# Kernel optimization log

Measured on AMD Instinct MI355X. Metric: run time of the kernel, lower is better.

Reference implementation:

```python
import jax, jax.numpy as jnp
import numpy as np

H = 64          # hidden_dim
NH = 4          # n_heads
DH = H // NH
F_OWN = 40      # own feature dim
FA = 24         # ally feature dim
FE = 24         # enemy feature dim
NAL = 15        # n_allies
NEN = 16        # n_enemies
BS = 2048       # episode batch
NAG = 16        # n_agents
BN = BS * NAG
AMOVE = 6       # normal (move) actions
HYPER_OUT = F_OWN * H + H + 4


def setup_inputs():
    key = jax.random.key(0)
    ks = jax.random.split(key, 32)
    g = lambda k, sh, s=1.0: jax.random.normal(k, sh, dtype=jnp.float32) * s
    inv = lambda d: float(1.0 / np.sqrt(d))
    return {
        "own_raw": g(ks[0], (BN, 1, F_OWN)),
        "ally_raw": g(ks[1], (BN, NAL, FA)),
        "enemy_raw": g(ks[2], (BN, NEN, FE)),
        "hidden_state": g(ks[3], (BN, H)),
        "hyp_W1": g(ks[4], (F_OWN, H), inv(F_OWN)),
        "hyp_b1": jnp.zeros((H,), jnp.float32),
        "hyp_W2": g(ks[5], (H, HYPER_OUT), 0.01 * inv(H)),  # torch init mul_(0.01)
        "hyp_b2": jnp.zeros((HYPER_OUT,), jnp.float32),
        "Wa": g(ks[6], (FA, H), inv(FA)), "ba": jnp.zeros((H,), jnp.float32),
        "We": g(ks[7], (FE, H), inv(FE)), "be": jnp.zeros((H,), jnp.float32),
        "aWq": g(ks[8], (H, H), inv(H)), "aWk": g(ks[9], (H, H), inv(H)),
        "aWv": g(ks[10], (H, H), inv(H)), "aWo": g(ks[11], (H, H), inv(H)),
        "eWq": g(ks[12], (H, H), inv(H)), "eWk": g(ks[13], (H, H), inv(H)),
        "eWv": g(ks[14], (H, H), inv(H)), "eWo": g(ks[15], (H, H), inv(H)),
        "gru_Wih": g(ks[16], (3 * H, 3 * H), inv(3 * H)),
        "gru_Whh": g(ks[17], (H, 3 * H), inv(H)),
        "gru_bih": jnp.zeros((3 * H,), jnp.float32),
        "gru_bhh": jnp.zeros((3 * H,), jnp.float32),
        "Wm": g(ks[18], (H, AMOVE), inv(H)), "bm": jnp.zeros((AMOVE,), jnp.float32),
        "WzK": g(ks[19], (H, H), inv(H)),
        "WEK": g(ks[20], (H, H), inv(H)),
        "bs": BS,
    }


def _mha(q_in, kv, mask, Wq, Wk, Wv, Wo):
    # masked multi-head cross attention: q_in [B,H], kv [B,n,H], mask [B,n] bool
    B, n = kv.shape[0], kv.shape[1]
    q = (q_in @ Wq).reshape(B, NH, DH)
    k = (kv @ Wk).reshape(B, n, NH, DH)
    v = (kv @ Wv).reshape(B, n, NH, DH)
    scores = jnp.einsum('bhd,bnhd->bhn', q, k) * float(1.0 / np.sqrt(DH))
    scores = jnp.where(mask[:, None, :], scores, -1e9)
    attn = jax.nn.softmax(scores, axis=-1)
    out = jnp.einsum('bhn,bnhd->bhd', attn, v).reshape(B, H)
    return out @ Wo


def reference(own_raw, ally_raw, enemy_raw, hidden_state,
              hyp_W1, hyp_b1, hyp_W2, hyp_b2,
              Wa, ba, We, be,
              aWq, aWk, aWv, aWo, eWq, eWk, eWv, eWo,
              gru_Wih, gru_Whh, gru_bih, gru_bhh,
              Wm, bm, WzK, WEK, bs):
    Bn = own_raw.shape[0]
    ally_mask = jnp.any(ally_raw != 0, axis=-1)    # ~all(x==0)
    enemy_mask = jnp.any(enemy_raw != 0, axis=-1)
    own_vec = own_raw[:, 0, :]                     # [Bn, F_OWN]
    # hypernet: per-agent own-embedding weights + bias (last 4 outputs unused, as in source)
    h_out = jax.nn.relu(own_vec @ hyp_W1 + hyp_b1) @ hyp_W2 + hyp_b2
    W_flat = h_out[:, :F_OWN * H].reshape(Bn, F_OWN, H)
    b_own = h_out[:, F_OWN * H:F_OWN * H + H]
    own_e = jnp.einsum('bf,bfh->bh', own_vec, W_flat) + b_own
    ally_e = ally_raw @ Wa + ba
    enemy_e = enemy_raw @ We + be
    zA = _mha(own_e, ally_e, ally_mask, aWq, aWk, aWv, aWo)
    zE = _mha(own_e, enemy_e, enemy_mask, eWq, eWk, eWv, eWo)
    u_cat = jnp.concatenate([own_e, zA, zE], axis=-1)  # [Bn, 3H]
    # GRUCell (torch semantics)
    gx = u_cat @ gru_Wih + gru_bih
    gh = hidden_state @ gru_Whh + gru_bhh
    xr, xz, xn = jnp.split(gx, 3, axis=-1)
    hr, hz, hn = jnp.split(gh, 3, axis=-1)
    r = jax.nn.sigmoid(xr + hr)
    zg = jax.nn.sigmoid(xz + hz)
    ncand = jnp.tanh(xn + r * hn)
    z = (1.0 - zg) * ncand + zg * hidden_state
    logits_move = z @ Wm + bm
    zk = z @ WzK
    Ek = enemy_e @ WEK
    logits_shoot = jnp.einsum('bd,bmd->bm', zk, Ek)
    Q = jnp.concatenate([logits_move, logits_shoot], axis=-1)[:, None, :]
    return Q, z.reshape(bs, -1, H)
```

## Files before the change

kernel.cpp:

```cpp
#include <hip/hip_runtime.h>
#include <hip/hip_bf16.h>
#include <math.h>

#define TB 32
#define LOG2E 1.44269504f

typedef float f32x4 __attribute__((ext_vector_type(4)));
typedef _Float16 f16x8 __attribute__((ext_vector_type(8)));
typedef _Float16 f16x4 __attribute__((ext_vector_type(4)));
typedef _Float16 f16x2 __attribute__((ext_vector_type(2)));

#define OFF_W1T  344064
#define OFF_WOA  352256
#define OFF_WOE  360448
#define OFF_VBA  368640
#define OFF_VBE  372736
#define OFF_GA   376832
#define OFF_GE   393216
#define OFF_GIH  409600
#define OFF_GHH  483328
#define OFF_GBS  507904
#define OFF_GBH  508672
#define OFF_BHD  508928

#define MFH(a, b, c) __builtin_amdgcn_mfma_f32_16x16x32_f16((a), (b), (c), 0, 0, 0)

__device__ inline float dot2(f16x2 a, f16x2 b, float c) {
#if __has_builtin(__builtin_amdgcn_fdot2)
  return __builtin_amdgcn_fdot2(a, b, c, false);
#else
  return c + (float)a[0] * (float)b[0] + (float)a[1] * (float)b[1];
#endif
}
__device__ inline f16x2 pk2(float x, float y) {
  f16x2 r; r[0] = (_Float16)x; r[1] = (_Float16)y; return r;
}

__global__ __launch_bounds__(256)
void prep_kernel(const float* __restrict__ hyp_W1, const float* __restrict__ hyp_b1,
                 const float* __restrict__ hyp_W2, const float* __restrict__ hyp_b2,
                 const float* __restrict__ Wa, const float* __restrict__ ba,
                 const float* __restrict__ We, const float* __restrict__ be,
                 const float* __restrict__ aWq, const float* __restrict__ aWk,
                 const float* __restrict__ aWv, const float* __restrict__ aWo,
                 const float* __restrict__ eWq, const float* __restrict__ eWk,
                 const float* __restrict__ eWv, const float* __restrict__ eWo,
                 const float* __restrict__ gWih, const float* __restrict__ gWhh,
                 const float* __restrict__ gbih, const float* __restrict__ gbhh,
                 const float* __restrict__ WzK, const float* __restrict__ WEK,
                 const float* __restrict__ Wm,
                 void* __restrict__ ws)
{
  const int b = blockIdx.x, t = threadIdx.x;
  if (b < 42) {
    _Float16* o = (_Float16*)ws;
    for (int i = t; i < 4096; i += 256) {
      int h = i >> 6, k = i & 63;
      float v;
      if (b < 40)       v = hyp_W2[(size_t)k * 2628 + b * 64 + h];
      else if (b == 40) v = hyp_W2[(size_t)k * 2628 + 2560 + h];
      else              v = (k < 40) ? hyp_b2[k * 64 + h]
                             : (k == 40 ? hyp_b2[2560 + h] : 0.0f);
      o[b * 4096 + i] = (_Float16)v;
    }
  } else if (b == 42) {
    _Float16* o = (_Float16*)((char*)ws + OFF_W1T);
    for (int i = t; i < 4096; i += 256) {
      int h = i >> 6, k = i & 63;
      float v = (k < 40) ? hyp_W1[k * 64 + h] : (k == 40 ? hyp_b1[h] : 0.0f);
      o[i] = (_Float16)v;
    }
  } else if (b == 43 || b == 44) {
    const float* M = (b == 43) ? aWo : eWo;
    _Float16* o = (_Float16*)((char*)ws + (b == 43 ? OFF_WOA : OFF_WOE));
    for (int i = t; i < 4096; i += 256)
      o[i] = (_Float16)M[(i & 63) * 64 + (i >> 6)];
  } else if (b == 45 || b == 46) {
    const float* Wemb = (b == 45) ? Wa : We;
    const float* bemb = (b == 45) ? ba : be;
    const float* Wv   = (b == 45) ? aWv : eWv;
    _Float16* o = (_Float16*)((char*)ws + (b == 45 ? OFF_VBA : OFF_VBE));
    for (int i = t; i < 2048; i += 256) {
      int h = i >> 5, k = i & 31;
      float v = 0.f;
      if (k < 24)       { for (int d = 0; d < 64; ++d) v += Wemb[k * 64 + d] * Wv[d * 64 + h]; }
      else if (k == 24) { for (int d = 0; d < 64; ++d) v += bemb[d] * Wv[d * 64 + h]; }
      o[i] = (_Float16)v;
    }
  } else if (b == 47 || b == 48) {
    const float* Wemb = (b == 47) ? Wa : We;
    const float* bemb = (b == 47) ? ba : be;
    const float* Wk   = (b == 47) ? aWk : eWk;
    const float* Wq   = (b == 47) ? aWq : eWq;
    _Float16* o = (_Float16*)((char*)ws + (b == 47 ? OFF_GA : OFF_GE));
    __shared__ float sKb[25 * 64];
    for (int i = t; i < 1600; i += 256) {
      int k = i >> 6, c = i & 63;
      float v = 0.f;
      if (k < 24)  { for (int d = 0; d < 64; ++d) v += Wemb[k * 64 + d] * Wk[d * 64 + c]; }
      else         { for (int d = 0; d < 64; ++d) v += bemb[d] * Wk[d * 64 + c]; }
      sKb[i] = v;
    }
    __syncthreads();
    for (int i = t; i < 8192; i += 256) {
      int col = i >> 6, d = i & 63;
      int h = col >> 5, kk = col & 31;
      float v = 0.f;
      if (kk < 25)
        for (int dh = 0; dh < 16; ++dh)
          v += Wq[d * 64 + h * 16 + dh] * sKb[kk * 64 + h * 16 + dh];
      o[i] = (_Float16)(v * 0.25f * LOG2E);
    }
  } else if (b == 49) {
    _Float16* o = (_Float16*)((char*)ws + OFF_GIH);
    for (int i = t; i < 36864; i += 256) {
      int d = i / 192, c = i - d * 192;
      o[c * 192 + d] = (_Float16)gWih[i];
    }
  } else if (b == 50) {
    _Float16* o = (_Float16*)((char*)ws + OFF_GHH);
    for (int i = t; i < 12288; i += 256) {
      int d = i / 192, c = i - d * 192;
      o[c * 64 + d] = (_Float16)gWhh[i];
    }
  } else if (b == 51) {
    float* gbS = (float*)((char*)ws + OFF_GBS);
    float* gbH = (float*)((char*)ws + OFF_GBH);
    if (t < 192) gbS[t] = gbih[t] + (t < 128 ? gbhh[t] : 0.0f);
    if (t < 64)  gbH[t] = gbhh[128 + t];
  } else if (b == 52) {
    __shared__ float sWsK[24 * 64];
    __shared__ float sbw[64];
    _Float16* o = (_Float16*)((char*)ws + OFF_BHD);
    for (int i = t; i < 1536; i += 256) {
      int j = i >> 6, h = i & 63;
      float v = 0.f;
      for (int c = 0; c < 64; ++c) v += We[j * 64 + c] * WEK[c * 64 + h];
      sWsK[i] = v;
    }
    if (t < 64) {
      float v = 0.f;
      for (int c = 0; c < 64; ++c) v += be[c] * WEK[c * 64 + t];
      sbw[t] = v;
    }
    __syncthreads();
    for (int i = t; i < 2048; i += 256) {
      int col = i >> 6, c = i & 63;
      float v = 0.f;
      if (col < 24)       { for (int d = 0; d < 64; ++d) v += WzK[c * 64 + d] * sWsK[col * 64 + d]; }
      else if (col == 24) { for (int d = 0; d < 64; ++d) v += WzK[c * 64 + d] * sbw[d]; }
      else if (col < 31)  v = Wm[c * 6 + (col - 25)];
      o[i] = (_Float16)v;
    }
  }
}

#define SCORE_BODY(Q0,Q1,Q2,Q3,Q4,Q5,WP,SCV)                                  \
  {                                                                            \
    unsigned orv =                                                             \
      ((Q0.x!=0.f)|(Q0.y!=0.f)|(Q0.z!=0.f)|(Q0.w!=0.f)|                        \
       (Q1.x!=0.f)|(Q1.y!=0.f)|(Q1.z!=0.f)|(Q1.w!=0.f)|                        \
       (Q2.x!=0.f)|(Q2.y!=0.f)|(Q2.z!=0.f)|(Q2.w!=0.f)|                        \
       (Q3.x!=0.f)|(Q3.y!=0.f)|(Q3.z!=0.f)|(Q3.w!=0.f)|                        \
       (Q4.x!=0.f)|(Q4.y!=0.f)|(Q4.z!=0.f)|(Q4.w!=0.f)|                        \
       (Q5.x!=0.f)|(Q5.y!=0.f)|(Q5.z!=0.f)|(Q5.w!=0.f)) ? 1u : 0u;             \
    f16x2 r0 = pk2(Q0.x,Q0.y), r1 = pk2(Q0.z,Q0.w);                            \
    f16x2 r2 = pk2(Q1.x,Q1.y), r3 = pk2(Q1.z,Q1.w);                            \
    f16x2 r4 = pk2(Q2.x,Q2.y), r5 = pk2(Q2.z,Q2.w);                            \
    f16x2 r6 = pk2(Q3.x,Q3.y), r7 = pk2(Q3.z,Q3.w);                            \
    f16x2 r8 = pk2(Q4.x,Q4.y), r9 = pk2(Q4.z,Q4.w);                            \
    f16x2 r10 = pk2(Q5.x,Q5.y), r11 = pk2(Q5.z,Q5.w);                          \
    _Pragma("unroll")                                                          \
    for (int h = 0; h < 4; ++h) {                                              \
      const _Float16* wq = (WP) + h * 32;                                      \
      float a = (float)wq[24];                                                 \
      a = dot2(r0,  *(const f16x2*)(wq + 0),  a);                              \
      a = dot2(r1,  *(const f16x2*)(wq + 2),  a);                              \
      a = dot2(r2,  *(const f16x2*)(wq + 4),  a);                              \
      a = dot2(r3,  *(const f16x2*)(wq + 6),  a);                              \
      a = dot2(r4,  *(const f16x2*)(wq + 8),  a);                              \
      a = dot2(r5,  *(const f16x2*)(wq + 10), a);                              \
      a = dot2(r6,  *(const f16x2*)(wq + 12), a);                              \
      a = dot2(r7,  *(const f16x2*)(wq + 14), a);                              \
      a = dot2(r8,  *(const f16x2*)(wq + 16), a);                              \
      a = dot2(r9,  *(const f16x2*)(wq + 18), a);                              \
      a = dot2(r10, *(const f16x2*)(wq + 20), a);                              \
      a = dot2(r11, *(const f16x2*)(wq + 22), a);                              \
      SCV[h] = orv ? a : -1.0e9f;                                              \
    }                                                                          \
  }

__global__ __launch_bounds__(256, 4)
void agent_kernel(
    const float* __restrict__ own_raw, const float* __restrict__ ally_raw,
    const float* __restrict__ enemy_raw, const float* __restrict__ hidden,
    const float* __restrict__ bm,
    const void* __restrict__ ws,
    float* __restrict__ out, int BN)
{
  __shared__ __align__(16) char s_all[37632];
  _Float16* s_u16 = (_Float16*)s_all;
  char*     sR2   = s_all + 12544;
  _Float16* s_own16 = (_Float16*)sR2;
  _Float16* s_ownT  = (_Float16*)(sR2 + 3328);
  _Float16* s_h116  = (_Float16*)(sR2 + 5888);
  _Float16* s_w0    = (_Float16*)sR2;
  _Float16* s_w1    = (_Float16*)(sR2 + 8320);
  _Float16* s_pp0   = (_Float16*)(sR2 + 16640);
  _Float16* s_pp1   = (_Float16*)(sR2 + 20864);
  _Float16* s_att0  = (_Float16*)sR2;
  _Float16* s_att1  = (_Float16*)(sR2 + 8320);
  _Float16* s_hid16 = (_Float16*)(sR2 + 16640);
  _Float16* s_z16   = (_Float16*)sR2;
  _Float16* s_t16   = (_Float16*)(sR2 + 4352);
  float*    s_q     = (float*)(sR2 + 8320);

  const int tid = threadIdx.x;
  const int bs0 = blockIdx.x * TB;
  const int l   = tid & 63;
  const int wv  = tid >> 6;
  const int lr  = l & 15;
  const int oct = l >> 4;
  const int s8  = tid >> 3;
  const int sh  = tid & 7;

  const f16x8 ZERO8F = {0,0,0,0,0,0,0,0};
  f16x8 ONE8F = ZERO8F; ONE8F[0] = (_Float16)1.0f;
  const f32x4 ZERO4 = {0.f, 0.f, 0.f, 0.f};

  for (int i = tid; i < 640; i += 256) {
    int ss = i / 20, c = i - ss * 20;
    float2 v = *(const float2*)(own_raw + (size_t)(bs0 + ss) * 40 + c * 2);
    *(f16x2*)(s_own16 + ss * 52 + c * 2) = pk2(v.x, v.y);
  }
  for (int i = tid; i < 1280; i += 256) {
    int f = i >> 5, s2 = i & 31;
    s_ownT[i] = (_Float16)own_raw[(size_t)(bs0 + s2) * 40 + f];
  }
  __syncthreads();

  {
    const _Float16* w1t = (const _Float16*)((const char*)ws + OFF_W1T);
    f16x8 b0 = *(const f16x8*)(w1t + (wv * 16 + lr) * 64 + oct * 8);
    f16x8 b1 = *(const f16x8*)(w1t + (wv * 16 + lr) * 64 + 32 + oct * 8);
    #pragma unroll
    for (int rt = 0; rt < 2; ++rt) {
      f16x8 a0 = *(const f16x8*)(s_own16 + (rt * 16 + lr) * 52 + oct * 8);
      f16x8 a1;
      if (oct == 0)      a1 = *(const f16x8*)(s_own16 + (rt * 16 + lr) * 52 + 32);
      else if (oct == 1) a1 = ONE8F;
      else               a1 = ZERO8F;
      f32x4 acc = ZERO4;
      acc = MFH(a0, b0, acc);
      acc = MFH(a1, b1, acc);
      #pragma unroll
      for (int j = 0; j < 4; ++j)
        s_h116[(rt * 16 + oct * 4 + j) * 68 + wv * 16 + lr] = (_Float16)fmaxf(acc[j], 0.f);
    }
  }
  __syncthreads();

  {
    const _Float16* bb = (const _Float16*)ws + (size_t)(wv * 16 + lr) * 64 + oct * 8;
    f16x8 h0f0 = *(const f16x8*)(s_h116 + lr * 68 + oct * 8);
    f16x8 h1f0 = *(const f16x8*)(s_h116 + lr * 68 + 32 + oct * 8);
    f16x8 h0f1 = *(const f16x8*)(s_h116 + (16 + lr) * 68 + oct * 8);
    f16x8 h1f1 = *(const f16x8*)(s_h116 + (16 + lr) * 68 + 32 + oct * 8);
    f32x4 acc0 = ZERO4, acc1 = ZERO4;
    #pragma unroll 4
    for (int f = 0; f < 40; ++f) {
      f16x8 b0 = *(const f16x8*)(bb + (size_t)f * 4096);
      f16x8 b1 = *(const f16x8*)(bb + (size_t)f * 4096 + 32);
      f32x4 y0 = MFH(h0f0, b0, ZERO4); y0 = MFH(h1f0, b1, y0);
      f32x4 y1 = MFH(h0f1, b0, ZERO4); y1 = MFH(h1f1, b1, y1);
      f16x4 ov0 = *(const f16x4*)(s_ownT + f * 32 + oct * 4);
      f16x4 ov1 = *(const f16x4*)(s_ownT + f * 32 + 16 + oct * 4);
      #pragma unroll
      for (int j = 0; j < 4; ++j) {
        acc0[j] += (float)ov0[j] * y0[j];
        acc1[j] += (float)ov1[j] * y1[j];
      }
    }
    f32x4 aD0 = ZERO4, aD1 = ZERO4;
    {
      f16x8 b0 = *(const f16x8*)(bb + (size_t)40 * 4096);
      f16x8 b1 = *(const f16x8*)(bb + (size_t)40 * 4096 + 32);
      aD0 = MFH(h0f0, b0, aD0); aD0 = MFH(h1f0, b1, aD0);
      aD1 = MFH(h0f1, b0, aD1); aD1 = MFH(h1f1, b1, aD1);
    }
    {
      f16x8 b0 = *(const f16x8*)(bb + (size_t)41 * 4096);
      f16x8 b1 = *(const f16x8*)(bb + (size_t)41 * 4096 + 32);
      #pragma unroll
      for (int rt = 0; rt < 2; ++rt) {
        f16x8 a0 = *(const f16x8*)(s_own16 + (rt * 16 + lr) * 52 + oct * 8);
        f16x8 a1;
        if (oct == 0)      a1 = *(const f16x8*)(s_own16 + (rt * 16 + lr) * 52 + 32);
        else if (oct == 1) a1 = ONE8F;
        else               a1 = ZERO8F;
        if (rt) { aD1 = MFH(a0, b0, aD1); aD1 = MFH(a1, b1, aD1); }
        else    { aD0 = MFH(a0, b0, aD0); aD0 = MFH(a1, b1, aD0); }
      }
    }
    #pragma unroll
    for (int j = 0; j < 4; ++j) {
      s_u16[(oct * 4 + j) * 196 + wv * 16 + lr]      = (_Float16)(acc0[j] + aD0[j]);
      s_u16[(16 + oct * 4 + j) * 196 + wv * 16 + lr] = (_Float16)(acc1[j] + aD1[j]);
    }
  }
  __syncthreads();

  {
    f16x8 a00 = *(const f16x8*)(s_u16 + lr * 196 + oct * 8);
    f16x8 a10 = *(const f16x8*)(s_u16 + lr * 196 + 32 + oct * 8);
    f16x8 a01 = *(const f16x8*)(s_u16 + (16 + lr) * 196 + oct * 8);
    f16x8 a11 = *(const f16x8*)(s_u16 + (16 + lr) * 196 + 32 + oct * 8);
    #pragma unroll
    for (int side = 0; side < 2; ++side) {
      const _Float16* gT = (const _Float16*)((const char*)ws + (side ? OFF_GE : OFF_GA));
      _Float16* wDst = side ? s_w1 : s_w0;
      #pragma unroll
      for (int t2 = 0; t2 < 2; ++t2) {
        int col = wv * 32 + t2 * 16 + lr;
        f16x8 b0 = *(const f16x8*)(gT + col * 64 + oct * 8);
        f16x8 b1 = *(const f16x8*)(gT + col * 64 + 32 + oct * 8);
        f32x4 ac0 = ZERO4, ac1 = ZERO4;
        ac0 = MFH(a00, b0, ac0); ac0 = MFH(a10, b1, ac0);
        ac1 = MFH(a01, b0, ac1); ac1 = MFH(a11, b1, ac1);
        #pragma unroll
        for (int j = 0; j < 4; ++j) {
          wDst[(oct * 4 + j) * 130 + col]      = (_Float16)ac0[j];
          wDst[(16 + oct * 4 + j) * 130 + col] = (_Float16)ac1[j];
        }
      }
    }
  }
  __syncthreads();

  {
    #pragma unroll
    for (int side = 0; side < 2; ++side) {
      const int n_ent = side ? 16 : 15;
      const int rstr  = side ? 384 : 360;
      const float* rawg = side ? enemy_raw : ally_raw;
      const _Float16* wp = (side ? s_w1 : s_w0) + s8 * 130;
      _Float16* pp = side ? s_pp1 : s_pp0;

      const int n1 = (sh + 8 < n_ent) ? (sh + 8) : (n_ent - 1);
      const float* rp0 = rawg + (size_t)(bs0 + s8) * rstr + sh * 24;
      const float* rp1 = rawg + (size_t)(bs0 + s8) * rstr + n1 * 24;
      float4 qa0 = *(const float4*)(rp0);      float4 qa1 = *(const float4*)(rp0 + 4);
      float4 qa2 = *(const float4*)(rp0 + 8);  float4 qa3 = *(const float4*)(rp0 + 12);
      float4 qa4 = *(const float4*)(rp0 + 16); float4 qa5 = *(const float4*)(rp0 + 20);
      float4 qb0 = *(const float4*)(rp1);      float4 qb1 = *(const float4*)(rp1 + 4);
      float4 qb2 = *(const float4*)(rp1 + 8);  float4 qb3 = *(const float4*)(rp1 + 12);
      float4 qb4 = *(const float4*)(rp1 + 16); float4 qb5 = *(const float4*)(rp1 + 20);

      f32x4 sc0, sc1;
      SCORE_BODY(qa0, qa1, qa2, qa3, qa4, qa5, wp, sc0);
      SCORE_BODY(qb0, qb1, qb2, qb3, qb4, qb5, wp, sc1);
      if (sh + 8 >= n_ent) {
        #pragma unroll
        for (int h = 0; h < 4; ++h) sc1[h] = -2.0e9f;
      }
      f32x4 m, lsum, p0v, p1v;
      #pragma unroll
      for (int h = 0; h < 4; ++h) m[h] = fmaxf(sc0[h], sc1[h]);
      #pragma unroll
      for (int d = 1; d < 8; d <<= 1) {
        #pragma unroll
        for (int h = 0; h < 4; ++h) m[h] = fmaxf(m[h], __shfl_xor(m[h], d));
      }
      #pragma unroll
      for (int h = 0; h < 4; ++h) {
        p0v[h] = __builtin_exp2f(sc0[h] - m[h]);
        p1v[h] = __builtin_exp2f(sc1[h] - m[h]);
        lsum[h] = p0v[h] + p1v[h];
      }
      #pragma unroll
      for (int d = 1; d < 8; d <<= 1) {
        #pragma unroll
        for (int h = 0; h < 4; ++h) lsum[h] += __shfl_xor(lsum[h], d);
      }
      f32x4 rl;
      #pragma unroll
      for (int h = 0; h < 4; ++h) rl[h] = __builtin_amdgcn_rcpf(lsum[h]);
      {
        f16x4 pk;
        #pragma unroll
        for (int h = 0; h < 4; ++h) pk[h] = (_Float16)(p0v[h] * rl[h]);
        *(f16x4*)(pp + sh * 132 + s8 * 4) = pk;
      }
      if (sh + 8 < n_ent) {
        f16x4 pk;
        #pragma unroll
        for (int h = 0; h < 4; ++h) pk[h] = (_Float16)(p1v[h] * rl[h]);
        *(f16x4*)(pp + (sh + 8) * 132 + s8 * 4) = pk;
      }
    }
  }
  __syncthreads();

  {
    #pragma unroll
    for (int side = 0; side < 2; ++side) {
      const int n_ent = side ? 16 : 15;
      const int rstr  = side ? 384 : 360;
      const float* rawg = side ? enemy_raw : ally_raw;
      const _Float16* vbT = (const _Float16*)((const char*)ws + (side ? OFF_VBE : OFF_VBA));
      const _Float16* pp = side ? s_pp1 : s_pp0;
      _Float16* attD = side ? s_att1 : s_att0;

      f16x8 vbF = *(const f16x8*)(vbT + (wv * 16 + lr) * 32 + oct * 8);
      const float* rpv0 = rawg + (size_t)(bs0 + lr) * rstr + oct * 8;
      const float* rpv1 = rawg + (size_t)(bs0 + 16 + lr) * rstr + oct * 8;
      f32x4 oac0 = ZERO4, oac1 = ZERO4;
      #pragma unroll
      for (int i = 0; i < 16; ++i) {
        if (i >= n_ent) break;
        _Float16 pw0 = pp[i * 132 + lr * 4 + wv];
        _Float16 pw1 = pp[i * 132 + (16 + lr) * 4 + wv];
        f16x8 fr0, fr1;
        if (oct < 3) {
          float4 a = *(const float4*)(rpv0 + i * 24);
          float4 b = *(const float4*)(rpv0 + i * 24 + 4);
          fr0[0] = (_Float16)a.x * pw0; fr0[1] = (_Float16)a.y * pw0;
          fr0[2] = (_Float16)a.z * pw0; fr0[3] = (_Float16)a.w * pw0;
          fr0[4] = (_Float16)b.x * pw0; fr0[5] = (_Float16)b.y * pw0;
          fr0[6] = (_Float16)b.z * pw0; fr0[7] = (_Float16)b.w * pw0;
          float4 c = *(const float4*)(rpv1 + i * 24);
          float4 d = *(const float4*)(rpv1 + i * 24 + 4);
          fr1[0] = (_Float16)c.x * pw1; fr1[1] = (_Float16)c.y * pw1;
          fr1[2] = (_Float16)c.z * pw1; fr1[3] = (_Float16)c.w * pw1;
          fr1[4] = (_Float16)d.x * pw1; fr1[5] = (_Float16)d.y * pw1;
          fr1[6] = (_Float16)d.z * pw1; fr1[7] = (_Float16)d.w * pw1;
        } else {
          fr0 = ZERO8F; fr0[0] = pw0;
          fr1 = ZERO8F; fr1[0] = pw1;
        }
        oac0 = MFH(fr0, vbF, oac0);
        oac1 = MFH(fr1, vbF, oac1);
      }
      if (side == 0) __syncthreads();
      #pragma unroll
      for (int j = 0; j < 4; ++j) {
        attD[(oct * 4 + j) * 68 + wv * 16 + lr]      = (_Float16)oac0[j];
        attD[(16 + oct * 4 + j) * 68 + wv * 16 + lr] = (_Float16)oac1[j];
      }
    }
  }
  __syncthreads();

  {
    #pragma unroll
    for (int side = 0; side < 2; ++side) {
      const _Float16* woT = (const _Float16*)((const char*)ws + (side ? OFF_WOE : OFF_WOA));
      const _Float16* attS = side ? s_att1 : s_att0;
      f16x8 b0 = *(const f16x8*)(woT + (wv * 16 + lr) * 64 + oct * 8);
      f16x8 b1 = *(const f16x8*)(woT + (wv * 16 + lr) * 64 + 32 + oct * 8);
      #pragma unroll
      for (int rt = 0; rt < 2; ++rt) {
        f16x8 a0 = *(const f16x8*)(attS + (rt * 16 + lr) * 68 + oct * 8);
        f16x8 a1 = *(const f16x8*)(attS + (rt * 16 + lr) * 68 + 32 + oct * 8);
        f32x4 oa = ZERO4;
        oa = MFH(a0, b0, oa);
        oa = MFH(a1, b1, oa);
        #pragma unroll
        for (int j = 0; j < 4; ++j)
          s_u16[(rt * 16 + oct * 4 + j) * 196 + 64 + side * 64 + wv * 16 + lr] = (_Float16)oa[j];
      }
    }
    for (int i = tid; i < 1024; i += 256) {
      int ss = i >> 5, c = i & 31;
      float2 v = *(const float2*)(hidden + (size_t)(bs0 + ss) * 64 + c * 2);
      *(f16x2*)(s_hid16 + ss * 68 + c * 2) = pk2(v.x, v.y);
    }
  }
  __syncthreads();

  {
    const _Float16* ihT = (const _Float16*)((const char*)ws + OFF_GIH);
    const _Float16* hhT = (const _Float16*)((const char*)ws + OFF_GHH);
    const float* gbS = (const float*)((const char*)ws + OFF_GBS);
    const float* gbH = (const float*)((const char*)ws + OFF_GBH);
    f32x4 aX0[2] = {ZERO4, ZERO4}, aX1[2] = {ZERO4, ZERO4};
    f32x4 aX2[2] = {ZERO4, ZERO4}, aH2[2] = {ZERO4, ZERO4};
    #pragma unroll
    for (int st = 0; st < 6; ++st) {
      f16x8 uf0 = *(const f16x8*)(s_u16 + lr * 196 + st * 32 + oct * 8);
      f16x8 uf1 = *(const f16x8*)(s_u16 + (16 + lr) * 196 + st * 32 + oct * 8);
      f16x8 b0 = *(const f16x8*)(ihT + ((wv    ) * 16 + lr) * 192 + st * 32 + oct * 8);
      f16x8 b1 = *(const f16x8*)(ihT + ((wv + 4) * 16 + lr) * 192 + st * 32 + oct * 8);
      f16x8 b2 = *(const f16x8*)(ihT + ((wv + 8) * 16 + lr) * 192 + st * 32 + oct * 8);
      aX0[0] = MFH(uf0, b0, aX0[0]);  aX0[1] = MFH(uf1, b0, aX0[1]);
      aX1[0] = MFH(uf0, b1, aX1[0]);  aX1[1] = MFH(uf1, b1, aX1[1]);
      aX2[0] = MFH(uf0, b2, aX2[0]);  aX2[1] = MFH(uf1, b2, aX2[1]);
    }
    #pragma unroll
    for (int st = 0; st < 2; ++st) {
      f16x8 hf0 = *(const f16x8*)(s_hid16 + lr * 68 + st * 32 + oct * 8);
      f16x8 hf1 = *(const f16x8*)(s_hid16 + (16 + lr) * 68 + st * 32 + oct * 8);
      f16x8 b0 = *(const f16x8*)(hhT + ((wv    ) * 16 + lr) * 64 + st * 32 + oct * 8);
      f16x8 b1 = *(const f16x8*)(hhT + ((wv + 4) * 16 + lr) * 64 + st * 32 + oct * 8);
      f16x8 b2 = *(const f16x8*)(hhT + ((wv + 8) * 16 + lr) * 64 + st * 32 + oct * 8);
      aX0[0] = MFH(hf0, b0, aX0[0]);  aX0[1] = MFH(hf1, b0, aX0[1]);
      aX1[0] = MFH(hf0, b1, aX1[0]);  aX1[1] = MFH(hf1, b1, aX1[1]);
      aH2[0] = MFH(hf0, b2, aH2[0]);  aH2[1] = MFH(hf1, b2, aH2[1]);
    }
    const int c0 = wv * 16 + lr;
    float bb0 = gbS[c0], bb1 = gbS[c0 + 64], bb2 = gbS[c0 + 128], bbh = gbH[c0];
    #pragma unroll
    for (int rt = 0; rt < 2; ++rt) {
      #pragma unroll
      for (int j = 0; j < 4; ++j) {
        int row = rt * 16 + oct * 4 + j;
        float xr = aX0[rt][j] + bb0;
        float xz = aX1[rt][j] + bb1;
        float xn = aX2[rt][j] + bb2;
        float hn = aH2[rt][j] + bbh;
        float r  = __builtin_amdgcn_rcpf(1.f + __builtin_exp2f(-xr * LOG2E));
        float zg = __builtin_amdgcn_rcpf(1.f + __builtin_exp2f(-xz * LOG2E));
        float ta = xn + r * hn;
        float nc = 1.f - 2.f * __builtin_amdgcn_rcpf(1.f + __builtin_exp2f(2.f * LOG2E * ta));
        float hv = (float)s_hid16[row * 68 + c0];
        s_z16[row * 68 + c0] = (_Float16)((1.f - zg) * nc + zg * hv);
      }
    }
  }
  __syncthreads();

  {
    const _Float16* bhT = (const _Float16*)((const char*)ws + OFF_BHD);
    const int rt = wv >> 1;
    const int col = (wv & 1) * 16 + lr;
    f16x8 a0 = *(const f16x8*)(s_z16 + (rt * 16 + lr) * 68 + oct * 8);
    f16x8 a1 = *(const f16x8*)(s_z16 + (rt * 16 + lr) * 68 + 32 + oct * 8);
    f16x8 b0 = *(const f16x8*)(bhT + col * 64 + oct * 8);
    f16x8 b1 = *(const f16x8*)(bhT + col * 64 + 32 + oct * 8);
    f32x4 td = ZERO4;
    td = MFH(a0, b0, td);
    td = MFH(a1, b1, td);
    #pragma unroll
    for (int j = 0; j < 4; ++j) {
      int row = rt * 16 + oct * 4 + j;
      if (col < 25)      s_t16[row * 26 + col] = (_Float16)td[j];
      else if (col < 31) s_q[row * 22 + (col - 25)] = td[j] + bm[col - 25];
    }
  }
  __syncthreads();
  {
    const _Float16* tp = s_t16 + s8 * 26;
    #pragma unroll
    for (int e = 0; e < 2; ++e) {
      int m = sh + e * 8;
      const float* er = enemy_raw + (size_t)(bs0 + s8) * 384 + m * 24;
      float acc2 = (float)tp[24];
      #pragma unroll
      for (int k4 = 0; k4 < 6; ++k4) {
        float4 r4 = *(const float4*)(er + k4 * 4);
        acc2 += r4.x * (float)tp[k4*4]   + r4.y * (float)tp[k4*4+1]
              + r4.z * (float)tp[k4*4+2] + r4.w * (float)tp[k4*4+3];
      }
      s_q[s8 * 22 + 6 + m] = acc2;
    }
  }
  __syncthreads();
  for (int i = tid; i < 704; i += 256)
    out[(size_t)bs0 * 22 + i] = s_q[i];
  for (int i = tid; i < 2048; i += 256)
    out[(size_t)BN * 22 + (size_t)bs0 * 64 + i] = (float)s_z16[(i >> 6) * 68 + (i & 63)];
}

extern "C" void kernel_launch(void* const* d_in, const int* in_sizes, int n_in,
                              void* d_out, int out_size, void* d_ws, size_t ws_size,
                              hipStream_t stream) {
  (void)n_in; (void)out_size; (void)ws_size;
  const float* own_raw   = (const float*)d_in[0];
  const float* ally_raw  = (const float*)d_in[1];
  const float* enemy_raw = (const float*)d_in[2];
  const float* hidden    = (const float*)d_in[3];
  const float* hyp_W1    = (const float*)d_in[4];
  const float* hyp_b1    = (const float*)d_in[5];
  const float* hyp_W2    = (const float*)d_in[6];
  const float* hyp_b2    = (const float*)d_in[7];
  const float* Wa        = (const float*)d_in[8];
  const float* ba        = (const float*)d_in[9];
  const float* We        = (const float*)d_in[10];
  const float* be        = (const float*)d_in[11];
  const float* aWq       = (const float*)d_in[12];
  const float* aWk       = (const float*)d_in[13];
  const float* aWv       = (const float*)d_in[14];
  const float* aWo       = (const float*)d_in[15];
  const float* eWq       = (const float*)d_in[16];
  const float* eWk       = (const float*)d_in[17];
  const float* eWv       = (const float*)d_in[18];
  const float* eWo       = (const float*)d_in[19];
  const float* gWih      = (const float*)d_in[20];
  const float* gWhh      = (const float*)d_in[21];
  const float* gbih      = (const float*)d_in[22];
  const float* gbhh      = (const float*)d_in[23];
  const float* Wm        = (const float*)d_in[24];
  const float* bm        = (const float*)d_in[25];
  const float* WzK       = (const float*)d_in[26];
  const float* WEK       = (const float*)d_in[27];
  int BN = in_sizes[0] / 40;
  int blocks = BN / TB;

  hipLaunchKernelGGL(prep_kernel, dim3(53), dim3(256), 0, stream,
                     hyp_W1, hyp_b1, hyp_W2, hyp_b2, Wa, ba, We, be,
                     aWq, aWk, aWv, aWo, eWq, eWk, eWv, eWo,
                     gWih, gWhh, gbih, gbhh, WzK, WEK, Wm, d_ws);
  hipLaunchKernelGGL(agent_kernel, dim3(blocks), dim3(256), 0, stream,
                     own_raw, ally_raw, enemy_raw, hidden, bm,
                     d_ws, (float*)d_out, BN);
}
```

Before: 146.7 us.

## Repad LDS strides, vectorize score dots, and make entity loops branch-free

Row strides of every shared-memory tile are padded to multiples of 8 halfs (52→56, 68→72, 130→136, 196→200), so 16-byte f16x8 loads are aligned and bank mapping changes. The attention score code now loads each weight row once as f16x8 vectors and reuses it for both entity slots. The final shoot logits convert the enemy rows to fp16 and use packed dot2 instead of scalar fp32 multiply-adds. The entity loop in the value aggregation loses its early break and uses clamped indices, and the probability scaling is done in fp32 before packing. One barrier is moved and s_q is relocated to a new region, which changes synchronisation and adds a small amount of LDS.

```diff
diff --git a/kernel.cpp b/kernel.cpp
--- a/kernel.cpp
+++ b/kernel.cpp
@@ -35,6 +35,30 @@
 __device__ inline f16x2 pk2(float x, float y) {
   f16x2 r; r[0] = (_Float16)x; r[1] = (_Float16)y; return r;
 }
+
+#define SV2(W, q) __builtin_shufflevector((W), (W), 2*(q), 2*(q)+1)
+
+#define CVT12(Q0,Q1,Q2,Q3,Q4,Q5,R) \
+  f16x2 R##_0=pk2(Q0.x,Q0.y), R##_1=pk2(Q0.z,Q0.w), \
+        R##_2=pk2(Q1.x,Q1.y), R##_3=pk2(Q1.z,Q1.w), \
+        R##_4=pk2(Q2.x,Q2.y), R##_5=pk2(Q2.z,Q2.w), \
+        R##_6=pk2(Q3.x,Q3.y), R##_7=pk2(Q3.z,Q3.w), \
+        R##_8=pk2(Q4.x,Q4.y), R##_9=pk2(Q4.z,Q4.w), \
+        R##_10=pk2(Q5.x,Q5.y), R##_11=pk2(Q5.z,Q5.w)
+
+#define ORV6(Q0,Q1,Q2,Q3,Q4,Q5) \
+  ((Q0.x!=0.f)|(Q0.y!=0.f)|(Q0.z!=0.f)|(Q0.w!=0.f)| \
+   (Q1.x!=0.f)|(Q1.y!=0.f)|(Q1.z!=0.f)|(Q1.w!=0.f)| \
+   (Q2.x!=0.f)|(Q2.y!=0.f)|(Q2.z!=0.f)|(Q2.w!=0.f)| \
+   (Q3.x!=0.f)|(Q3.y!=0.f)|(Q3.z!=0.f)|(Q3.w!=0.f)| \
+   (Q4.x!=0.f)|(Q4.y!=0.f)|(Q4.z!=0.f)|(Q4.w!=0.f)| \
+   (Q5.x!=0.f)|(Q5.y!=0.f)|(Q5.z!=0.f)|(Q5.w!=0.f))
+
+#define DOT12(R, WA, WB, WC, BIAS) \
+  dot2(R##_11, SV2(WC,3), dot2(R##_10, SV2(WC,2), dot2(R##_9, SV2(WC,1), dot2(R##_8, SV2(WC,0), \
+  dot2(R##_7,  SV2(WB,3), dot2(R##_6,  SV2(WB,2), dot2(R##_5, SV2(WB,1), dot2(R##_4, SV2(WB,0), \
+  dot2(R##_3,  SV2(WA,3), dot2(R##_2,  SV2(WA,2), dot2(R##_1, SV2(WA,1), dot2(R##_0, SV2(WA,0), \
+  (BIAS)))))))))))))
 
 __global__ __launch_bounds__(256)
 void prep_kernel(const float* __restrict__ hyp_W1, const float* __restrict__ hyp_b1,
@@ -155,41 +179,6 @@
   }
 }
 
-#define SCORE_BODY(Q0,Q1,Q2,Q3,Q4,Q5,WP,SCV)                                  \
-  {                                                                            \
-    unsigned orv =                                                             \
-      ((Q0.x!=0.f)|(Q0.y!=0.f)|(Q0.z!=0.f)|(Q0.w!=0.f)|                        \
-       (Q1.x!=0.f)|(Q1.y!=0.f)|(Q1.z!=0.f)|(Q1.w!=0.f)|                        \
-       (Q2.x!=0.f)|(Q2.y!=0.f)|(Q2.z!=0.f)|(Q2.w!=0.f)|                        \
-       (Q3.x!=0.f)|(Q3.y!=0.f)|(Q3.z!=0.f)|(Q3.w!=0.f)|                        \
-       (Q4.x!=0.f)|(Q4.y!=0.f)|(Q4.z!=0.f)|(Q4.w!=0.f)|                        \
-       (Q5.x!=0.f)|(Q5.y!=0.f)|(Q5.z!=0.f)|(Q5.w!=0.f)) ? 1u : 0u;             \
-    f16x2 r0 = pk2(Q0.x,Q0.y), r1 = pk2(Q0.z,Q0.w);                            \
-    f16x2 r2 = pk2(Q1.x,Q1.y), r3 = pk2(Q1.z,Q1.w);                            \
-    f16x2 r4 = pk2(Q2.x,Q2.y), r5 = pk2(Q2.z,Q2.w);                            \
-    f16x2 r6 = pk2(Q3.x,Q3.y), r7 = pk2(Q3.z,Q3.w);                            \
-    f16x2 r8 = pk2(Q4.x,Q4.y), r9 = pk2(Q4.z,Q4.w);                            \
-    f16x2 r10 = pk2(Q5.x,Q5.y), r11 = pk2(Q5.z,Q5.w);                          \
-    _Pragma("unroll")                                                          \
-    for (int h = 0; h < 4; ++h) {                                              \
-      const _Float16* wq = (WP) + h * 32;                                      \
-      float a = (float)wq[24];                                                 \
-      a = dot2(r0,  *(const f16x2*)(wq + 0),  a);                              \
-      a = dot2(r1,  *(const f16x2*)(wq + 2),  a);                              \
-      a = dot2(r2,  *(const f16x2*)(wq + 4),  a);                              \
-      a = dot2(r3,  *(const f16x2*)(wq + 6),  a);                              \
-      a = dot2(r4,  *(const f16x2*)(wq + 8),  a);                              \
-      a = dot2(r5,  *(const f16x2*)(wq + 10), a);                              \
-      a = dot2(r6,  *(const f16x2*)(wq + 12), a);                              \
-      a = dot2(r7,  *(const f16x2*)(wq + 14), a);                              \
-      a = dot2(r8,  *(const f16x2*)(wq + 16), a);                              \
-      a = dot2(r9,  *(const f16x2*)(wq + 18), a);                              \
-      a = dot2(r10, *(const f16x2*)(wq + 20), a);                              \
-      a = dot2(r11, *(const f16x2*)(wq + 22), a);                              \
-      SCV[h] = orv ? a : -1.0e9f;                                              \
-    }                                                                          \
-  }
-
 __global__ __launch_bounds__(256, 4)
 void agent_kernel(
     const float* __restrict__ own_raw, const float* __restrict__ ally_raw,
@@ -198,22 +187,22 @@
     const void* __restrict__ ws,
     float* __restrict__ out, int BN)
 {
-  __shared__ __align__(16) char s_all[37632];
+  __shared__ __align__(16) char s_all[38656];
   _Float16* s_u16 = (_Float16*)s_all;
-  char*     sR2   = s_all + 12544;
+  char*     sR2   = s_all + 12800;
   _Float16* s_own16 = (_Float16*)sR2;
-  _Float16* s_ownT  = (_Float16*)(sR2 + 3328);
-  _Float16* s_h116  = (_Float16*)(sR2 + 5888);
+  _Float16* s_ownT  = (_Float16*)(sR2 + 3584);
+  _Float16* s_h116  = (_Float16*)(sR2 + 6144);
   _Float16* s_w0    = (_Float16*)sR2;
-  _Float16* s_w1    = (_Float16*)(sR2 + 8320);
-  _Float16* s_pp0   = (_Float16*)(sR2 + 16640);
-  _Float16* s_pp1   = (_Float16*)(sR2 + 20864);
+  _Float16* s_w1    = (_Float16*)(sR2 + 8704);
+  _Float16* s_pp0   = (_Float16*)(sR2 + 17408);
+  _Float16* s_pp1   = (_Float16*)(sR2 + 21632);
   _Float16* s_att0  = (_Float16*)sR2;
-  _Float16* s_att1  = (_Float16*)(sR2 + 8320);
-  _Float16* s_hid16 = (_Float16*)(sR2 + 16640);
+  _Float16* s_att1  = (_Float16*)(sR2 + 8704);
+  _Float16* s_hid16 = (_Float16*)(sR2 + 17408);
   _Float16* s_z16   = (_Float16*)sR2;
-  _Float16* s_t16   = (_Float16*)(sR2 + 4352);
-  float*    s_q     = (float*)(sR2 + 8320);
+  _Float16* s_t16   = (_Float16*)(sR2 + 4608);
+  float*    s_q     = (float*)(sR2 + 17408);
 
   const int tid = threadIdx.x;
   const int bs0 = blockIdx.x * TB;
@@ -231,7 +220,7 @@
   for (int i = tid; i < 640; i += 256) {
     int ss = i / 20, c = i - ss * 20;
     float2 v = *(const float2*)(own_raw + (size_t)(bs0 + ss) * 40 + c * 2);
-    *(f16x2*)(s_own16 + ss * 52 + c * 2) = pk2(v.x, v.y);
+    *(f16x2*)(s_own16 + ss * 56 + c * 2) = pk2(v.x, v.y);
   }
   for (int i = tid; i < 1280; i += 256) {
     int f = i >> 5, s2 = i & 31;
@@ -245,9 +234,9 @@
     f16x8 b1 = *(const f16x8*)(w1t + (wv * 16 + lr) * 64 + 32 + oct * 8);
     #pragma unroll
     for (int rt = 0; rt < 2; ++rt) {
-      f16x8 a0 = *(const f16x8*)(s_own16 + (rt * 16 + lr) * 52 + oct * 8);
+      f16x8 a0 = *(const f16x8*)(s_own16 + (rt * 16 + lr) * 56 + oct * 8);
       f16x8 a1;
-      if (oct == 0)      a1 = *(const f16x8*)(s_own16 + (rt * 16 + lr) * 52 + 32);
+      if (oct == 0)      a1 = *(const f16x8*)(s_own16 + (rt * 16 + lr) * 56 + 32);
       else if (oct == 1) a1 = ONE8F;
       else               a1 = ZERO8F;
       f32x4 acc = ZERO4;
@@ -255,17 +244,17 @@
       acc = MFH(a1, b1, acc);
       #pragma unroll
       for (int j = 0; j < 4; ++j)
-        s_h116[(rt * 16 + oct * 4 + j) * 68 + wv * 16 + lr] = (_Float16)fmaxf(acc[j], 0.f);
+        s_h116[(rt * 16 + oct * 4 + j) * 72 + wv * 16 + lr] = (_Float16)fmaxf(acc[j], 0.f);
     }
   }
   __syncthreads();
 
   {
     const _Float16* bb = (const _Float16*)ws + (size_t)(wv * 16 + lr) * 64 + oct * 8;
-    f16x8 h0f0 = *(const f16x8*)(s_h116 + lr * 68 + oct * 8);
-    f16x8 h1f0 = *(const f16x8*)(s_h116 + lr * 68 + 32 + oct * 8);
-    f16x8 h0f1 = *(const f16x8*)(s_h116 + (16 + lr) * 68 + oct * 8);
-    f16x8 h1f1 = *(const f16x8*)(s_h116 + (16 + lr) * 68 + 32 + oct * 8);
+    f16x8 h0f0 = *(const f16x8*)(s_h116 + lr * 72 + oct * 8);
+    f16x8 h1f0 = *(const f16x8*)(s_h116 + lr * 72 + 32 + oct * 8);
+    f16x8 h0f1 = *(const f16x8*)(s_h116 + (16 + lr) * 72 + oct * 8);
+    f16x8 h1f1 = *(const f16x8*)(s_h116 + (16 + lr) * 72 + 32 + oct * 8);
     f32x4 acc0 = ZERO4, acc1 = ZERO4;
     #pragma unroll 4
     for (int f = 0; f < 40; ++f) {
@@ -293,9 +282,9 @@
       f16x8 b1 = *(const f16x8*)(bb + (size_t)41 * 4096 + 32);
       #pragma unroll
       for (int rt = 0; rt < 2; ++rt) {
-        f16x8 a0 = *(const f16x8*)(s_own16 + (rt * 16 + lr) * 52 + oct * 8);
+        f16x8 a0 = *(const f16x8*)(s_own16 + (rt * 16 + lr) * 56 + oct * 8);
         f16x8 a1;
-        if (oct == 0)      a1 = *(const f16x8*)(s_own16 + (rt * 16 + lr) * 52 + 32);
+        if (oct == 0)      a1 = *(const f16x8*)(s_own16 + (rt * 16 + lr) * 56 + 32);
         else if (oct == 1) a1 = ONE8F;
         else               a1 = ZERO8F;
         if (rt) { aD1 = MFH(a0, b0, aD1); aD1 = MFH(a1, b1, aD1); }
@@ -304,17 +293,17 @@
     }
     #pragma unroll
     for (int j = 0; j < 4; ++j) {
-      s_u16[(oct * 4 + j) * 196 + wv * 16 + lr]      = (_Float16)(acc0[j] + aD0[j]);
-      s_u16[(16 + oct * 4 + j) * 196 + wv * 16 + lr] = (_Float16)(acc1[j] + aD1[j]);
-    }
-  }
-  __syncthreads();
-
-  {
-    f16x8 a00 = *(const f16x8*)(s_u16 + lr * 196 + oct * 8);
-    f16x8 a10 = *(const f16x8*)(s_u16 + lr * 196 + 32 + oct * 8);
-    f16x8 a01 = *(const f16x8*)(s_u16 + (16 + lr) * 196 + oct * 8);
-    f16x8 a11 = *(const f16x8*)(s_u16 + (16 + lr) * 196 + 32 + oct * 8);
+      s_u16[(oct * 4 + j) * 200 + wv * 16 + lr]      = (_Float16)(acc0[j] + aD0[j]);
+      s_u16[(16 + oct * 4 + j) * 200 + wv * 16 + lr] = (_Float16)(acc1[j] + aD1[j]);
+    }
+  }
+  __syncthreads();
+
+  {
+    f16x8 a00 = *(const f16x8*)(s_u16 + lr * 200 + oct * 8);
+    f16x8 a10 = *(const f16x8*)(s_u16 + lr * 200 + 32 + oct * 8);
+    f16x8 a01 = *(const f16x8*)(s_u16 + (16 + lr) * 200 + oct * 8);
+    f16x8 a11 = *(const f16x8*)(s_u16 + (16 + lr) * 200 + 32 + oct * 8);
     #pragma unroll
     for (int side = 0; side < 2; ++side) {
       const _Float16* gT = (const _Float16*)((const char*)ws + (side ? OFF_GE : OFF_GA));
@@ -329,8 +318,8 @@
         ac1 = MFH(a01, b0, ac1); ac1 = MFH(a11, b1, ac1);
         #pragma unroll
         for (int j = 0; j < 4; ++j) {
-          wDst[(oct * 4 + j) * 130 + col]      = (_Float16)ac0[j];
-          wDst[(16 + oct * 4 + j) * 130 + col] = (_Float16)ac1[j];
+          wDst[(oct * 4 + j) * 136 + col]      = (_Float16)ac0[j];
+          wDst[(16 + oct * 4 + j) * 136 + col] = (_Float16)ac1[j];
         }
       }
     }
@@ -343,10 +332,10 @@
       const int n_ent = side ? 16 : 15;
       const int rstr  = side ? 384 : 360;
       const float* rawg = side ? enemy_raw : ally_raw;
-      const _Float16* wp = (side ? s_w1 : s_w0) + s8 * 130;
+      const _Float16* wp = (side ? s_w1 : s_w0) + s8 * 136;
       _Float16* pp = side ? s_pp1 : s_pp0;
 
-      const int n1 = (sh + 8 < n_ent) ? (sh + 8) : (n_ent - 1);
+      const int n1 = (sh + 8 < n_ent) ? (sh + 8) : 0;
       const float* rp0 = rawg + (size_t)(bs0 + s8) * rstr + sh * 24;
       const float* rp1 = rawg + (size_t)(bs0 + s8) * rstr + n1 * 24;
       float4 qa0 = *(const float4*)(rp0);      float4 qa1 = *(const float4*)(rp0 + 4);
@@ -355,10 +344,25 @@
       float4 qb0 = *(const float4*)(rp1);      float4 qb1 = *(const float4*)(rp1 + 4);
       float4 qb2 = *(const float4*)(rp1 + 8);  float4 qb3 = *(const float4*)(rp1 + 12);
       float4 qb4 = *(const float4*)(rp1 + 16); float4 qb5 = *(const float4*)(rp1 + 20);
+      unsigned oa = ORV6(qa0, qa1, qa2, qa3, qa4, qa5);
+      unsigned ob = ORV6(qb0, qb1, qb2, qb3, qb4, qb5);
+      CVT12(qa0, qa1, qa2, qa3, qa4, qa5, ra);
+      f16x8 w0a = *(const f16x8*)(wp +  0), w0b = *(const f16x8*)(wp +  8), w0c = *(const f16x8*)(wp + 16);
+      f16x8 w1a = *(const f16x8*)(wp + 32), w1b = *(const f16x8*)(wp + 40), w1c = *(const f16x8*)(wp + 48);
+      f16x8 w2a = *(const f16x8*)(wp + 64), w2b = *(const f16x8*)(wp + 72), w2c = *(const f16x8*)(wp + 80);
+      f16x8 w3a = *(const f16x8*)(wp + 96), w3b = *(const f16x8*)(wp +104), w3c = *(const f16x8*)(wp +112);
+      float bi0 = (float)wp[24], bi1 = (float)wp[56], bi2 = (float)wp[88], bi3 = (float)wp[120];
 
       f32x4 sc0, sc1;
-      SCORE_BODY(qa0, qa1, qa2, qa3, qa4, qa5, wp, sc0);
-      SCORE_BODY(qb0, qb1, qb2, qb3, qb4, qb5, wp, sc1);
+      sc0[0] = oa ? DOT12(ra, w0a, w0b, w0c, bi0) : -1.0e9f;
+      sc0[1] = oa ? DOT12(ra, w1a, w1b, w1c, bi1) : -1.0e9f;
+      sc0[2] = oa ? DOT12(ra, w2a, w2b, w2c, bi2) : -1.0e9f;
+      sc0[3] = oa ? DOT12(ra, w3a, w3b, w3c, bi3) : -1.0e9f;
+      CVT12(qb0, qb1, qb2, qb3, qb4, qb5, rb);
+      sc1[0] = ob ? DOT12(rb, w0a, w0b, w0c, bi0) : -1.0e9f;
+      sc1[1] = ob ? DOT12(rb, w1a, w1b, w1c, bi1) : -1.0e9f;
+      sc1[2] = ob ? DOT12(rb, w2a, w2b, w2c, bi2) : -1.0e9f;
+      sc1[3] = ob ? DOT12(rb, w3a, w3b, w3c, bi3) : -1.0e9f;
       if (sh + 8 >= n_ent) {
         #pragma unroll
         for (int h = 0; h < 4; ++h) sc1[h] = -2.0e9f;
@@ -391,7 +395,7 @@
         for (int h = 0; h < 4; ++h) pk[h] = (_Float16)(p0v[h] * rl[h]);
         *(f16x4*)(pp + sh * 132 + s8 * 4) = pk;
       }
-      if (sh + 8 < n_ent) {
+      {
         f16x4 pk;
         #pragma unroll
         for (int h = 0; h < 4; ++h) pk[h] = (_Float16)(p1v[h] * rl[h]);
@@ -417,35 +421,32 @@
       f32x4 oac0 = ZERO4, oac1 = ZERO4;
       #pragma unroll
       for (int i = 0; i < 16; ++i) {
-        if (i >= n_ent) break;
-        _Float16 pw0 = pp[i * 132 + lr * 4 + wv];
-        _Float16 pw1 = pp[i * 132 + (16 + lr) * 4 + wv];
+        const int ii = (i < n_ent) ? i : 0;
+        float pwf0 = (float)pp[i * 132 + lr * 4 + wv];
+        float pwf1 = (float)pp[i * 132 + (16 + lr) * 4 + wv];
         f16x8 fr0, fr1;
         if (oct < 3) {
-          float4 a = *(const float4*)(rpv0 + i * 24);
-          float4 b = *(const float4*)(rpv0 + i * 24 + 4);
-          fr0[0] = (_Float16)a.x * pw0; fr0[1] = (_Float16)a.y * pw0;
-          fr0[2] = (_Float16)a.z * pw0; fr0[3] = (_Float16)a.w * pw0;
-          fr0[4] = (_Float16)b.x * pw0; fr0[5] = (_Float16)b.y * pw0;
-          fr0[6] = (_Float16)b.z * pw0; fr0[7] = (_Float16)b.w * pw0;
-          float4 c = *(const float4*)(rpv1 + i * 24);
-          float4 d = *(const float4*)(rpv1 + i * 24 + 4);
-          fr1[0] = (_Float16)c.x * pw1; fr1[1] = (_Float16)c.y * pw1;
-          fr1[2] = (_Float16)c.z * pw1; fr1[3] = (_Float16)c.w * pw1;
-          fr1[4] = (_Float16)d.x * pw1; fr1[5] = (_Float16)d.y * pw1;
-          fr1[6] = (_Float16)d.z * pw1; fr1[7] = (_Float16)d.w * pw1;
+          float4 a = *(const float4*)(rpv0 + ii * 24);
+          float4 b = *(const float4*)(rpv0 + ii * 24 + 4);
+          f16x4 lo0 = __builtin_shufflevector(pk2(a.x*pwf0, a.y*pwf0), pk2(a.z*pwf0, a.w*pwf0), 0,1,2,3);
+          f16x4 hi0 = __builtin_shufflevector(pk2(b.x*pwf0, b.y*pwf0), pk2(b.z*pwf0, b.w*pwf0), 0,1,2,3);
+          fr0 = __builtin_shufflevector(lo0, hi0, 0,1,2,3,4,5,6,7);
+          float4 c = *(const float4*)(rpv1 + ii * 24);
+          float4 d = *(const float4*)(rpv1 + ii * 24 + 4);
+          f16x4 lo1 = __builtin_shufflevector(pk2(c.x*pwf1, c.y*pwf1), pk2(c.z*pwf1, c.w*pwf1), 0,1,2,3);
+          f16x4 hi1 = __builtin_shufflevector(pk2(d.x*pwf1, d.y*pwf1), pk2(d.z*pwf1, d.w*pwf1), 0,1,2,3);
+          fr1 = __builtin_shufflevector(lo1, hi1, 0,1,2,3,4,5,6,7);
         } else {
-          fr0 = ZERO8F; fr0[0] = pw0;
-          fr1 = ZERO8F; fr1[0] = pw1;
+          fr0 = ZERO8F; fr0[0] = (_Float16)pwf0;
+          fr1 = ZERO8F; fr1[0] = (_Float16)pwf1;
         }
         oac0 = MFH(fr0, vbF, oac0);
         oac1 = MFH(fr1, vbF, oac1);
       }
-      if (side == 0) __syncthreads();
       #pragma unroll
       for (int j = 0; j < 4; ++j) {
-        attD[(oct * 4 + j) * 68 + wv * 16 + lr]      = (_Float16)oac0[j];
-        attD[(16 + oct * 4 + j) * 68 + wv * 16 + lr] = (_Float16)oac1[j];
+        attD[(oct * 4 + j) * 72 + wv * 16 + lr]      = (_Float16)oac0[j];
+        attD[(16 + oct * 4 + j) * 72 + wv * 16 + lr] = (_Float16)oac1[j];
       }
     }
   }
@@ -460,20 +461,20 @@
       f16x8 b1 = *(const f16x8*)(woT + (wv * 16 + lr) * 64 + 32 + oct * 8);
       #pragma unroll
       for (int rt = 0; rt < 2; ++rt) {
-        f16x8 a0 = *(const f16x8*)(attS + (rt * 16 + lr) * 68 + oct * 8);
-        f16x8 a1 = *(const f16x8*)(attS + (rt * 16 + lr) * 68 + 32 + oct * 8);
+        f16x8 a0 = *(const f16x8*)(attS + (rt * 16 + lr) * 72 + oct * 8);
+        f16x8 a1 = *(const f16x8*)(attS + (rt * 16 + lr) * 72 + 32 + oct * 8);
         f32x4 oa = ZERO4;
         oa = MFH(a0, b0, oa);
         oa = MFH(a1, b1, oa);
         #pragma unroll
         for (int j = 0; j < 4; ++j)
-          s_u16[(rt * 16 + oct * 4 + j) * 196 + 64 + side * 64 + wv * 16 + lr] = (_Float16)oa[j];
+          s_u16[(rt * 16 + oct * 4 + j) * 200 + 64 + side * 64 + wv * 16 + lr] = (_Float16)oa[j];
       }
     }
     for (int i = tid; i < 1024; i += 256) {
       int ss = i >> 5, c = i & 31;
       float2 v = *(const float2*)(hidden + (size_t)(bs0 + ss) * 64 + c * 2);
-      *(f16x2*)(s_hid16 + ss * 68 + c * 2) = pk2(v.x, v.y);
+      *(f16x2*)(s_hid16 + ss * 72 + c * 2) = pk2(v.x, v.y);
     }
   }
   __syncthreads();
@@ -487,8 +488,8 @@
     f32x4 aX2[2] = {ZERO4, ZERO4}, aH2[2] = {ZERO4, ZERO4};
     #pragma unroll
     for (int st = 0; st < 6; ++st) {
-      f16x8 uf0 = *(const f16x8*)(s_u16 + lr * 196 + st * 32 + oct * 8);
-      f16x8 uf1 = *(const f16x8*)(s_u16 + (16 + lr) * 196 + st * 32 + oct * 8);
+      f16x8 uf0 = *(const f16x8*)(s_u16 + lr * 200 + st * 32 + oct * 8);
+      f16x8 uf1 = *(const f16x8*)(s_u16 + (16 + lr) * 200 + st * 32 + oct * 8);
       f16x8 b0 = *(const f16x8*)(ihT + ((wv    ) * 16 + lr) * 192 + st * 32 + oct * 8);
       f16x8 b1 = *(const f16x8*)(ihT + ((wv + 4) * 16 + lr) * 192 + st * 32 + oct * 8);
       f16x8 b2 = *(const f16x8*)(ihT + ((wv + 8) * 16 + lr) * 192 + st * 32 + oct * 8);
@@ -498,8 +499,8 @@
     }
     #pragma unroll
     for (int st = 0; st < 2; ++st) {
-      f16x8 hf0 = *(const f16x8*)(s_hid16 + lr * 68 + st * 32 + oct * 8);
-      f16x8 hf1 = *(const f16x8*)(s_hid16 + (16 + lr) * 68 + st * 32 + oct * 8);
+      f16x8 hf0 = *(const f16x8*)(s_hid16 + lr * 72 + st * 32 + oct * 8);
+      f16x8 hf1 = *(const f16x8*)(s_hid16 + (16 + lr) * 72 + st * 32 + oct * 8);
       f16x8 b0 = *(const f16x8*)(hhT + ((wv    ) * 16 + lr) * 64 + st * 32 + oct * 8);
       f16x8 b1 = *(const f16x8*)(hhT + ((wv + 4) * 16 + lr) * 64 + st * 32 + oct * 8);
       f16x8 b2 = *(const f16x8*)(hhT + ((wv + 8) * 16 + lr) * 64 + st * 32 + oct * 8);
@@ -509,6 +510,7 @@
     }
     const int c0 = wv * 16 + lr;
     float bb0 = gbS[c0], bb1 = gbS[c0 + 64], bb2 = gbS[c0 + 128], bbh = gbH[c0];
+    __syncthreads();
     #pragma unroll
     for (int rt = 0; rt < 2; ++rt) {
       #pragma unroll
@@ -522,8 +524,8 @@
         float zg = __builtin_amdgcn_rcpf(1.f + __builtin_exp2f(-xz * LOG2E));
         float ta = xn + r * hn;
         float nc = 1.f - 2.f * __builtin_amdgcn_rcpf(1.f + __builtin_exp2f(2.f * LOG2E * ta));
-        float hv = (float)s_hid16[row * 68 + c0];
-        s_z16[row * 68 + c0] = (_Float16)((1.f - zg) * nc + zg * hv);
+        float hv = (float)s_hid16[row * 72 + c0];
+        s_z16[row * 72 + c0] = (_Float16)((1.f - zg) * nc + zg * hv);
       }
     }
   }
@@ -533,8 +535,8 @@
     const _Float16* bhT = (const _Float16*)((const char*)ws + OFF_BHD);
     const int rt = wv >> 1;
     const int col = (wv & 1) * 16 + lr;
-    f16x8 a0 = *(const f16x8*)(s_z16 + (rt * 16 + lr) * 68 + oct * 8);
-    f16x8 a1 = *(const f16x8*)(s_z16 + (rt * 16 + lr) * 68 + 32 + oct * 8);
+    f16x8 a0 = *(const f16x8*)(s_z16 + (rt * 16 + lr) * 72 + oct * 8);
+    f16x8 a1 = *(const f16x8*)(s_z16 + (rt * 16 + lr) * 72 + 32 + oct * 8);
     f16x8 b0 = *(const f16x8*)(bhT + col * 64 + oct * 8);
     f16x8 b1 = *(const f16x8*)(bhT + col * 64 + 32 + oct * 8);
     f32x4 td = ZERO4;
@@ -543,32 +545,33 @@
     #pragma unroll
     for (int j = 0; j < 4; ++j) {
       int row = rt * 16 + oct * 4 + j;
-      if (col < 25)      s_t16[row * 26 + col] = (_Float16)td[j];
+      if (col < 25)      s_t16[row * 32 + col] = (_Float16)td[j];
       else if (col < 31) s_q[row * 22 + (col - 25)] = td[j] + bm[col - 25];
     }
   }
   __syncthreads();
   {
-    const _Float16* tp = s_t16 + s8 * 26;
+    const _Float16* tp = s_t16 + s8 * 32;
+    f16x8 t0 = *(const f16x8*)(tp);
+    f16x8 t1 = *(const f16x8*)(tp + 8);
+    f16x8 t2 = *(const f16x8*)(tp + 16);
+    float c24 = (float)tp[24];
     #pragma unroll
     for (int e = 0; e < 2; ++e) {
       int m = sh + e * 8;
       const float* er = enemy_raw + (size_t)(bs0 + s8) * 384 + m * 24;
-      float acc2 = (float)tp[24];
-      #pragma unroll
-      for (int k4 = 0; k4 < 6; ++k4) {
-        float4 r4 = *(const float4*)(er + k4 * 4);
-        acc2 += r4.x * (float)tp[k4*4]   + r4.y * (float)tp[k4*4+1]
-              + r4.z * (float)tp[k4*4+2] + r4.w * (float)tp[k4*4+3];
-      }
-      s_q[s8 * 22 + 6 + m] = acc2;
+      float4 q0 = *(const float4*)(er);      float4 q1 = *(const float4*)(er + 4);
+      float4 q2 = *(const float4*)(er + 8);  float4 q3 = *(const float4*)(er + 12);
+      float4 q4 = *(const float4*)(er + 16); float4 q5 = *(const float4*)(er + 20);
+      CVT12(q0, q1, q2, q3, q4, q5, rs);
+      s_q[s8 * 22 + 6 + m] = DOT12(rs, t0, t1, t2, c24);
     }
   }
   __syncthreads();
   for (int i = tid; i < 704; i += 256)
     out[(size_t)bs0 * 22 + i] = s_q[i];
   for (int i = tid; i < 2048; i += 256)
-    out[(size_t)BN * 22 + (size_t)bs0 * 64 + i] = (float)s_z16[(i >> 6) * 68 + (i & 63)];
+    out[(size_t)BN * 22 + (size_t)bs0 * 64 + i] = (float)s_z16[(i >> 6) * 72 + (i & 63)];
 }
 
 extern "C" void kernel_launch(void* const* d_in, const int* in_sizes, int n_in,
```

Measured after the change: 147.1 us. No clear change (+0.2%).
